# Optimization experiments

Hardware: AMD Instinct MI355X
Metric: run time of the kernel (lower is better)

## Reference

```python
import jax, jax.numpy as jnp
import numpy as np

# J2 (von Mises) elastic-plastic material, plane strain, linear isotropic hardening.
# State per integration point: committed strain (3), in-plane stress (3), out-of-plane
# stress szz (1), equivalent plastic strain eqps (1, the 'history' variable).
E_MOD = 3130.0   # Young's modulus (epoxy-like, MPa)
NU = 0.37        # Poisson ratio
SIGY0 = 64.8     # initial yield stress
HARD = 100.0     # linear hardening modulus
G_MOD = E_MOD / (2.0 * (1.0 + NU))
LAM = E_MOD * NU / ((1.0 + NU) * (1.0 - 2.0 * NU))


def _elastic_D():
    c = E_MOD / ((1.0 + NU) * (1.0 - 2.0 * NU))
    return jnp.array([[c * (1.0 - NU), c * NU, 0.0],
                      [c * NU, c * (1.0 - NU), 0.0],
                      [0.0, 0.0, G_MOD]], dtype=jnp.float32)


def _j2_step(carry, strain_t):
    # strain_t: [P,3] total strain (engineering shear) at this timestep
    eps_old, sig_old, szz_old, eqps = carry
    D = _elastic_D()
    deps = strain_t - eps_old
    sig_tr = sig_old + deps @ D.T                       # trial in-plane stress [P,3]
    szz_tr = szz_old + LAM * (deps[:, 0] + deps[:, 1])  # plane-strain out-of-plane stress
    p = (sig_tr[:, 0] + sig_tr[:, 1] + szz_tr) / 3.0
    dxx = sig_tr[:, 0] - p
    dyy = sig_tr[:, 1] - p
    dzz = szz_tr - p
    dxy = sig_tr[:, 2]
    q = jnp.sqrt(1.5 * (dxx * dxx + dyy * dyy + dzz * dzz + 2.0 * dxy * dxy) + 1e-12)
    f = q - (SIGY0 + HARD * eqps)
    dgam = jnp.where(f > 0.0, f / (3.0 * G_MOD + HARD), 0.0)  # radial return
    fac = 1.0 - 3.0 * G_MOD * dgam / q
    sig_new = jnp.stack([p + fac * dxx, p + fac * dyy, fac * dxy], axis=-1)
    szz_new = p + fac * dzz
    eqps_new = eqps + dgam  # commit()
    return (strain_t, sig_new, szz_new, eqps_new), sig_new


def reference(x, W1, W2):
    # x: [B,S,F]; W1: [ls,F] (fc1, no bias); W2: [O,ls] (softLayer: softplus-constrained weights)
    B, S, F = x.shape
    ls = W1.shape[0]
    bulk = ls // 3
    P = B * bulk
    # fc1 for all timesteps at once, then reshape to per-point strains [S, P, 3]
    strains = jnp.einsum('bsf,hf->bsh', x, W1)
    strains = strains.reshape(B, S, bulk, 3).transpose(1, 0, 2, 3).reshape(S, P, 3)
    init = (jnp.zeros((P, 3), jnp.float32), jnp.zeros((P, 3), jnp.float32),
            jnp.zeros((P,), jnp.float32), jnp.zeros((P,), jnp.float32))
    _, stresses = jax.lax.scan(_j2_step, init, strains)        # [S, P, 3]
    stresses = stresses.reshape(S, B, ls).transpose(1, 0, 2)   # [B, S, ls]
    out = jnp.einsum('bsh,oh->bso', stresses, jax.nn.softplus(W2))
    return out


def setup_inputs() -> dict:
    key = jax.random.key(0)
    k1, k2, k3 = jax.random.split(key, 3)
    B, S, F, ls, O = 128, 2048, 3, 192, 3
    x = jax.random.normal(k1, (B, S, F), dtype=jnp.float32) * 0.01  # strain-scale inputs
    W1 = jax.random.normal(k2, (ls, F), dtype=jnp.float32) / np.sqrt(F)
    W2 = jax.random.normal(k3, (O, ls), dtype=jnp.float32) / np.sqrt(ls)
    return {"x": x, "W1": W1, "W2": W2}
```

## Files before the change

### kernel.cpp

```cpp
#include <hip/hip_runtime.h>
#include <cmath>

namespace {
constexpr float kE   = 3130.0f;
constexpr float kNu  = 0.37f;
constexpr float kSy0 = 64.8f;
constexpr float kH   = 100.0f;
constexpr float kG   = kE / (2.0f * (1.0f + kNu));
constexpr float kLam = kE * kNu / ((1.0f + kNu) * (1.0f - 2.0f * kNu));
constexpr float kC   = kE / ((1.0f + kNu) * (1.0f - 2.0f * kNu));
constexpr float kC11 = kC * (1.0f - kNu);
constexpr float kC12 = kC * kNu;
constexpr float kC2  = 3.0f * kG / (3.0f * kG + kH);
constexpr float kC3  = kH / (3.0f * kG + kH);
constexpr int kS  = 2048;
constexpr int kT  = 16;
constexpr int kNBLK = kS / kT;
constexpr int kLs = 192;
constexpr float kSq15  = 1.224744871391589f;
constexpr float kSq3   = 1.732050807568877f;
constexpr float kISq15 = 1.0f / kSq15;
constexpr float kISq3  = 1.0f / kSq3;
}

typedef __fp16 half2_t __attribute__((ext_vector_type(2)));

__device__ __forceinline__ unsigned pk16(float a, float b) {
    half2_t h = __builtin_amdgcn_cvt_pkrtz(a, b);
    return __builtin_bit_cast(unsigned, h);
}
__device__ __forceinline__ float up16lo(unsigned u) {
    half2_t h = __builtin_bit_cast(half2_t, u);
    return (float)h.x;
}
__device__ __forceinline__ float up16hi(unsigned u) {
    half2_t h = __builtin_bit_cast(half2_t, u);
    return (float)h.y;
}

template<int CTRL, int RM, int BM>
__device__ __forceinline__ float dppmov(float v) {
    return __int_as_float(
        __builtin_amdgcn_update_dpp(0, __float_as_int(v), CTRL, RM, BM, false));
}
__device__ __forceinline__ float wave_sum63(float v) {
    v += dppmov<0x111, 0xf, 0xf>(v);
    v += dppmov<0x112, 0xf, 0xf>(v);
    v += dppmov<0x114, 0xf, 0xf>(v);
    v += dppmov<0x118, 0xf, 0xf>(v);
    v += dppmov<0x142, 0xa, 0xf>(v);
    v += dppmov<0x143, 0xc, 0xf>(v);
    return v;
}

__global__ __launch_bounds__(64, 1)
void j2_scan_stream(const float* __restrict__ x,
                    const float* __restrict__ W1,
                    uint4* __restrict__ ws)
{
    const int b = blockIdx.x;
    const int k = threadIdx.x;

    float wr[3][3];
#pragma unroll
    for (int j = 0; j < 3; ++j)
#pragma unroll
        for (int f = 0; f < 3; ++f)
            wr[j][f] = W1[(3 * k + j) * 3 + f];

    float g0[3], g1[3], e2s[3];
#pragma unroll
    for (int f = 0; f < 3; ++f) {
        const float e0 = kC11 * wr[0][f] + kC12 * wr[1][f];
        const float e1 = kC12 * wr[0][f] + kC11 * wr[1][f];
        const float lv = kLam * (wr[0][f] + wr[1][f]);
        g0[f]  = kSq15 * (2.0f * e0 - e1 - lv) * (1.0f / 3.0f);
        g1[f]  = kSq15 * (2.0f * e1 - e0 - lv) * (1.0f / 3.0f);
        e2s[f] = kSq3 * kG * wr[2][f];
    }

    const float* xb = x + (size_t)b * (kS * 3);

    float fw[52], fn[52];
    fw[0] = fw[1] = fw[2] = fw[3] = 0.0f;
    {
        const float4* s4 = reinterpret_cast<const float4*>(xb);
#pragma unroll
        for (int i = 0; i < 12; ++i) {
            float4 v = s4[i];
            fw[4 + 4 * i] = v.x; fw[5 + 4 * i] = v.y;
            fw[6 + 4 * i] = v.z; fw[7 + 4 * i] = v.w;
        }
    }

    float s0 = 0.f, s1 = 0.f, s2 = 0.f;
    float y = kSy0, c2y = kC2 * kSy0;
    uint4 st;

    for (int p = 0; p < kNBLK; ++p) {
        if (p + 1 < kNBLK) {
            const float4* s4 =
                reinterpret_cast<const float4*>(xb + 48 * (p + 1) - 4);
#pragma unroll
            for (int i = 0; i < 13; ++i) {
                float4 v = s4[i];
                fn[4 * i]     = v.x; fn[4 * i + 1] = v.y;
                fn[4 * i + 2] = v.z; fn[4 * i + 3] = v.w;
            }
        }
#pragma unroll
        for (int t = 0; t < kT; ++t) {
            const float d0 = fw[4 + 3 * t] - fw[1 + 3 * t];
            const float d1 = fw[5 + 3 * t] - fw[2 + 3 * t];
            const float d2 = fw[6 + 3 * t] - fw[3 + 3 * t];
            const float s0t = fmaf(g0[0], d0, fmaf(g0[1], d1, fmaf(g0[2], d2, s0)));
            const float s1t = fmaf(g1[0], d0, fmaf(g1[1], d1, fmaf(g1[2], d2, s1)));
            const float s2t = fmaf(e2s[0], d0, fmaf(e2s[1], d1, fmaf(e2s[2], d2, s2)));
            const float tt  = s0t + s1t;
            float a = fmaf(s0t, s0t, 1e-12f);
            a = fmaf(s1t, s1t, a);
            a = fmaf(s2t, s2t, a);
            const float q2  = fmaf(tt, tt, a);
            const float rq  = __builtin_amdgcn_rsqf(q2);
            const float fac = fminf(fmaf(c2y, rq, kC3), 1.0f);
            s0 = fac * s0t; s1 = fac * s1t; s2 = fac * s2t;
            const float qv = q2 * rq;
            y = fmaxf(y, fmaf(kC3, qv, c2y));
            c2y = kC2 * y;
            if ((t & 1) == 0) {
                st.x = pk16(s0, s1); st.y = pk16(s2, s2);
            } else {
                st.z = pk16(s0, s1); st.w = pk16(s2, s2);
                ws[((size_t)b * 1024 + p * 8 + (t >> 1)) * 64 + k] = st;
            }
        }
        if (p + 1 < kNBLK) {
#pragma unroll
            for (int i = 0; i < 52; ++i) fw[i] = fn[i];
        }
    }
}

__global__ __launch_bounds__(64, 1)
void j2_out_einsum(const float* __restrict__ x,
                   const float* __restrict__ W1,
                   const float* __restrict__ W2,
                   const uint4* __restrict__ ws,
                   float* __restrict__ out)
{
    const int b = blockIdx.x;
    const int tile = blockIdx.y;
    const int k = threadIdx.x;

    float wr[3][3];
#pragma unroll
    for (int j = 0; j < 3; ++j)
#pragma unroll
        for (int f = 0; f < 3; ++f)
            wr[j][f] = W1[(3 * k + j) * 3 + f];
    float mv[3];
#pragma unroll
    for (int f = 0; f < 3; ++f) {
        const float e0 = kC11 * wr[0][f] + kC12 * wr[1][f];
        const float e1 = kC12 * wr[0][f] + kC11 * wr[1][f];
        const float lv = kLam * (wr[0][f] + wr[1][f]);
        mv[f] = (e0 + e1 + lv) * (1.0f / 3.0f);
    }
    float spp[3][3], so[3];
#pragma unroll
    for (int o = 0; o < 3; ++o) {
        const float a0 = __logf(1.0f + __expf(W2[o * kLs + 3 * k + 0]));
        const float a1 = __logf(1.0f + __expf(W2[o * kLs + 3 * k + 1]));
        const float a2 = __logf(1.0f + __expf(W2[o * kLs + 3 * k + 2]));
        spp[o][0] = a0 * kISq15;
        spp[o][1] = a1 * kISq15;
        spp[o][2] = a2 * kISq3;
        so[o] = a0 + a1;
    }

    float fx[48];
    {
        const float4* s4 = reinterpret_cast<const float4*>(
            x + (size_t)b * (kS * 3) + tile * 48);
#pragma unroll
        for (int i = 0; i < 12; ++i) {
            float4 v = s4[i];
            fx[4 * i]     = v.x; fx[4 * i + 1] = v.y;
            fx[4 * i + 2] = v.z; fx[4 * i + 3] = v.w;
        }
    }

    float r[48];
#pragma unroll
    for (int j = 0; j < 8; ++j) {
        const uint4 v = ws[((size_t)b * 1024 + tile * 8 + j)* 64 + k];
#pragma unroll
        for (int h = 0; h < 2; ++h) {
            const int t = 2 * j + h;
            const unsigned pa = h ? v.z : v.x;
            const unsigned pb = h ? v.w : v.y;
            const float sx = up16lo(pa);
            const float sy = up16hi(pa);
            const float sv = up16lo(pb);
            const float pm = fmaf(mv[0], fx[3 * t],
                             fmaf(mv[1], fx[3 * t + 1], mv[2] * fx[3 * t + 2]));
#pragma unroll
            for (int o = 0; o < 3; ++o) {
                const float A = fmaf(spp[o][0], sx,
                                fmaf(spp[o][1], sy, spp[o][2] * sv));
                r[3 * t + o] = fmaf(pm, so[o], A);
            }
        }
    }
#pragma unroll
    for (int v = 0; v < 48; ++v) r[v] = wave_sum63(r[v]);
    if (k == 63) {
        float4* o4 = reinterpret_cast<float4*>(
            out + (size_t)b * (kS * 3) + tile * 48);
#pragma unroll
        for (int i = 0; i < 12; ++i)
            o4[i] = make_float4(r[4 * i], r[4 * i + 1],
                                r[4 * i + 2], r[4 * i + 3]);
    }
}

__global__ __launch_bounds__(192, 1)
void j2_pc_kernel(const float* __restrict__ x,
                  const float* __restrict__ W1,
                  const float* __restrict__ W2,
                  float* __restrict__ out)
{
    __shared__ float4 ubuf[2][kT][64];
    __shared__ float4 sgbuf[2][kT][64];

    const int b = blockIdx.x;
    const int w = threadIdx.x >> 6;
    const int k = threadIdx.x & 63;

    const float* xb = x + (size_t)b * (kS * 3);
    float* ob = out + (size_t)b * (kS * 3);

    float e0[3], e1[3], e2[3], lv[3], sp[3][3];
    if (w != 0) {
        float wr[3][3];
#pragma unroll
        for (int j = 0; j < 3; ++j)
#pragma unroll
            for (int f = 0; f < 3; ++f)
                wr[j][f] = W1[(3 * k + j) * 3 + f];
#pragma unroll
        for (int f = 0; f < 3; ++f) {
            e0[f] = kC11 * wr[0][f] + kC12 * wr[1][f];
            e1[f] = kC12 * wr[0][f] + kC11 * wr[1][f];
            e2[f] = kG * wr[2][f];
            lv[f] = kLam * (wr[0][f] + wr[1][f]);
        }
#pragma unroll
        for (int o = 0; o < 3; ++o)
#pragma unroll
            for (int j = 0; j < 3; ++j) {
                float v = W2[o * kLs + 3 * k + j];
                sp[o][j] = log1pf(expf(v));
            }
    }

    float sg0 = 0.f, sg1 = 0.f, sg2 = 0.f, szz = 0.f;
    float y = kSy0;
    const int tlo = (w == 2) ? 8 : 0;
    constexpr float kInv3GH = 1.0f / (3.0f * kG + kH);
    constexpr float k3G = 3.0f * kG;

    for (int phase = 0; phase <= kNBLK + 1; ++phase) {
        if (w == 0) {
            if (phase >= 1 && phase <= kNBLK) {
                const int blk = phase - 1, pb = blk & 1;
                float4 u[kT];
#pragma unroll
                for (int t = 0; t < kT; ++t) u[t] = ubuf[pb][t][k];
#pragma unroll
                for (int t = 0; t < kT; ++t) {
                    const float t0 = sg0 + u[t].x;
                    const float t1 = sg1 + u[t].y;
                    const float t2 = sg2 + u[t].z;
                    const float tz = szz + u[t].w;
                    const float pm  = (t0 + t1 + tz) * (1.0f / 3.0f);
                    const float dxx = t0 - pm, dyy = t1 - pm, dzz = tz - pm;
                    const float sa  = fmaf(dxx, dxx, dyy * dyy);
                    const float sb  = fmaf(dzz, dzz, (2.0f * t2) * t2);
                    const float q2  = fmaf(1.5f, sa + sb, 1e-12f);
                    const float qq  = __builtin_amdgcn_sqrtf(q2);
                    const float rq  = __builtin_amdgcn_rcpf(qq);
                    const float f   = qq - y;
                    const float dg  = (f > 0.0f) ? f * kInv3GH : 0.0f;
                    y = fmaf(kH, dg, y);
                    const float fac = fmaf(-(k3G * dg), rq, 1.0f);
                    sg0 = fmaf(fac, dxx, pm);
                    sg1 = fmaf(fac, dyy, pm);
                    sg2 = fac * t2;
                    szz = fmaf(fac, dzz, pm);
                    sgbuf[pb][t][k] = make_float4(sg0, sg1, sg2, 0.f);
                }
            }
        } else {
            if (phase < kNBLK) {
                const int p = phase, pb = p & 1;
                float xv[28];
                if (w == 1) {
                    if (p == 0) {
                        xv[0] = xv[1] = xv[2] = xv[3] = 0.f;
                        const float4* s4 = reinterpret_cast<const float4*>(xb);
#pragma unroll
                        for (int i = 0; i < 6; ++i) {
                            float4 v = s4[i];
                            xv[4 + 4 * i] = v.x; xv[5 + 4 * i] = v.y;
                            xv[6 + 4 * i] = v.z; xv[7 + 4 * i] = v.w;
                        }
                    } else {
                        const float4* s4 =
                            reinterpret_cast<const float4*>(xb + p * 48 - 4);
#pragma unroll
                        for (int i = 0; i < 7; ++i) {
                            float4 v = s4[i];
                            xv[4 * i]     = v.x; xv[4 * i + 1] = v.y;
                            xv[4 * i + 2] = v.z; xv[4 * i + 3] = v.w;
                        }
                    }
                } else {
                    const float4* s4 =
                        reinterpret_cast<const float4*>(xb + p * 48 + 20);
#pragma unroll
                    for (int i = 0; i < 7; ++i) {
                        float4 v = s4[i];
                        xv[4 * i]     = v.x; xv[4 * i + 1] = v.y;
                        xv[4 * i + 2] = v.z; xv[4 * i + 3] = v.w;
                    }
                }
                const int tbase = (w == 2) ? 8 : 0;
#pragma unroll
                for (int t = 0; t < 8; ++t) {
                    const float dx0 = xv[3 * t + 4] - xv[3 * t + 1];
                    const float dx1 = xv[3 * t + 5] - xv[3 * t + 2];
                    const float dx2 = xv[3 * t + 6] - xv[3 * t + 3];
                    float4 u;
                    u.x = fmaf(e0[0], dx0, fmaf(e0[1], dx1, e0[2] * dx2));
                    u.y = fmaf(e1[0], dx0, fmaf(e1[1], dx1, e1[2] * dx2));
                    u.z = fmaf(e2[0], dx0, fmaf(e2[1], dx1, e2[2] * dx2));
                    u.w = fmaf(lv[0], dx0, fmaf(lv[1], dx1, lv[2] * dx2));
                    ubuf[pb][tbase + t][k] = u;
                }
            }
            if (phase >= 2) {
                const int q = phase - 2, qb = q & 1;
                const int tbase = tlo;
                float r[24];
#pragma unroll
                for (int t = 0; t < 8; ++t) {
                    float4 s = sgbuf[qb][tbase + t][k];
                    r[3 * t]     = fmaf(sp[0][0], s.x, fmaf(sp[0][1], s.y, sp[0][2] * s.z));
                    r[3 * t + 1] = fmaf(sp[1][0], s.x, fmaf(sp[1][1], s.y, sp[1][2] * s.z));
                    r[3 * t + 2] = fmaf(sp[2][0], s.x, fmaf(sp[2][1], s.y, sp[2][2] * s.z));
                }
#pragma unroll
                for (int v = 0; v < 24; ++v) r[v] = wave_sum63(r[v]);
                if (k == 63) {
                    float4* o4 = reinterpret_cast<float4*>(ob + q * 48 + tbase * 3);
#pragma unroll
                    for (int i = 0; i < 6; ++i)
                        o4[i] = make_float4(r[4 * i], r[4 * i + 1],
                                            r[4 * i + 2], r[4 * i + 3]);
                }
            }
        }
        __syncthreads();
    }
}

extern "C" void kernel_launch(void* const* d_in, const int* in_sizes, int n_in,
                              void* d_out, int out_size, void* d_ws, size_t ws_size,
                              hipStream_t stream) {
    const float* x  = (const float*)d_in[0];
    const float* W1 = (const float*)d_in[1];
    const float* W2 = (const float*)d_in[2];
    float* out = (float*)d_out;

    const size_t need = (size_t)128 * 1024 * 64 * sizeof(uint4);
    if (ws_size >= need) {
        uint4* ws = (uint4*)d_ws;
        j2_scan_stream<<<dim3(128), dim3(64), 0, stream>>>(x, W1, ws);
        j2_out_einsum<<<dim3(128, 128), dim3(64), 0, stream>>>(x, W1, W2, ws, out);
    } else {
        j2_pc_kernel<<<dim3(128), dim3(192), 0, stream>>>(x, W1, W2, out);
    }
}
```

Before: 169.3 us.

## Precompute duplicated strain deltas and use packed FP32 math in scan

Adds a preprocessing kernel that computes per-timestep input differences and stores each one twice in a global buffer. The serial scan kernel then reads these with double-buffered vector loads and computes the two deviatoric stress components with packed v_pk_fma_f32 instructions. It also reorders the q² reduction to shorten the dependency chain. The aim is to cut per-step latency on the sequential critical path, at the cost of an extra kernel launch and about 6 MB of extra global memory traffic.

```diff
diff --git a/kernel.cpp b/kernel.cpp
--- a/kernel.cpp
+++ b/kernel.cpp
@@ -24,6 +24,8 @@
 }
 
 typedef __fp16 half2_t __attribute__((ext_vector_type(2)));
+typedef float f2_t __attribute__((ext_vector_type(2)));
+typedef float f4_t __attribute__((ext_vector_type(4)));
 
 __device__ __forceinline__ unsigned pk16(float a, float b) {
     half2_t h = __builtin_amdgcn_cvt_pkrtz(a, b);
@@ -36,6 +38,15 @@
 __device__ __forceinline__ float up16hi(unsigned u) {
     half2_t h = __builtin_bit_cast(half2_t, u);
     return (float)h.y;
+}
+
+__device__ __forceinline__ f2_t pkmul(f2_t a, f2_t b) {
+    f2_t d;
+    asm("v_pk_mul_f32 %0, %1, %2" : "=v"(d) : "v"(a), "v"(b));
+    return d;
+}
+__device__ __forceinline__ void pkfma(f2_t& acc, f2_t a, f2_t b) {
+    asm("v_pk_fma_f32 %0, %1, %2, %0" : "+v"(acc) : "v"(a), "v"(b));
 }
 
 template<int CTRL, int RM, int BM>
@@ -53,10 +64,26 @@
     return v;
 }
 
+__device__ __align__(16) float g_dxd[128 * 2048 * 6];
+
+__global__ __launch_bounds__(256, 4)
+void j2_dx_dup(const float* __restrict__ x)
+{
+    const int gid = blockIdx.x * 256 + threadIdx.x;
+    const int t = gid & 2047;
+    const float* xe = x + (size_t)gid * 3;
+    const float a0 = xe[0], a1 = xe[1], a2 = xe[2];
+    float p0 = 0.f, p1 = 0.f, p2 = 0.f;
+    if (t != 0) { p0 = xe[-3]; p1 = xe[-2]; p2 = xe[-1]; }
+    const float d0 = a0 - p0, d1 = a1 - p1, d2 = a2 - p2;
+    float2* o = reinterpret_cast<float2*>(g_dxd + (size_t)gid * 6);
+    o[0] = make_float2(d0, d0);
+    o[1] = make_float2(d1, d1);
+    o[2] = make_float2(d2, d2);
+}
+
 __global__ __launch_bounds__(64, 1)
-void j2_scan_stream(const float* __restrict__ x,
-                    const float* __restrict__ W1,
-                    uint4* __restrict__ ws)
+void j2_scan2(const float* __restrict__ W1, uint4* __restrict__ ws)
 {
     const int b = blockIdx.x;
     const int k = threadIdx.x;
@@ -68,77 +95,82 @@
         for (int f = 0; f < 3; ++f)
             wr[j][f] = W1[(3 * k + j) * 3 + f];
 
-    float g0[3], g1[3], e2s[3];
+    f2_t g01[3];
+    float e2s[3];
 #pragma unroll
     for (int f = 0; f < 3; ++f) {
         const float e0 = kC11 * wr[0][f] + kC12 * wr[1][f];
         const float e1 = kC12 * wr[0][f] + kC11 * wr[1][f];
         const float lv = kLam * (wr[0][f] + wr[1][f]);
-        g0[f]  = kSq15 * (2.0f * e0 - e1 - lv) * (1.0f / 3.0f);
-        g1[f]  = kSq15 * (2.0f * e1 - e0 - lv) * (1.0f / 3.0f);
-        e2s[f] = kSq3 * kG * wr[2][f];
-    }
-
-    const float* xb = x + (size_t)b * (kS * 3);
-
-    float fw[52], fn[52];
-    fw[0] = fw[1] = fw[2] = fw[3] = 0.0f;
-    {
-        const float4* s4 = reinterpret_cast<const float4*>(xb);
-#pragma unroll
-        for (int i = 0; i < 12; ++i) {
-            float4 v = s4[i];
-            fw[4 + 4 * i] = v.x; fw[5 + 4 * i] = v.y;
-            fw[6 + 4 * i] = v.z; fw[7 + 4 * i] = v.w;
-        }
-    }
+        g01[f][0] = kSq15 * (2.0f * e0 - e1 - lv) * (1.0f / 3.0f);
+        g01[f][1] = kSq15 * (2.0f * e1 - e0 - lv) * (1.0f / 3.0f);
+        e2s[f]    = kSq3 * kG * wr[2][f];
+    }
+
+    const float* db = g_dxd + (size_t)b * (2048 * 6);
 
     float s0 = 0.f, s1 = 0.f, s2 = 0.f;
     float y = kSy0, c2y = kC2 * kSy0;
-    uint4 st;
-
-    for (int p = 0; p < kNBLK; ++p) {
-        if (p + 1 < kNBLK) {
-            const float4* s4 =
-                reinterpret_cast<const float4*>(xb + 48 * (p + 1) - 4);
-#pragma unroll
-            for (int i = 0; i < 13; ++i) {
-                float4 v = s4[i];
-                fn[4 * i]     = v.x; fn[4 * i + 1] = v.y;
-                fn[4 * i + 2] = v.z; fn[4 * i + 3] = v.w;
-            }
-        }
-#pragma unroll
-        for (int t = 0; t < kT; ++t) {
-            const float d0 = fw[4 + 3 * t] - fw[1 + 3 * t];
-            const float d1 = fw[5 + 3 * t] - fw[2 + 3 * t];
-            const float d2 = fw[6 + 3 * t] - fw[3 + 3 * t];
-            const float s0t = fmaf(g0[0], d0, fmaf(g0[1], d1, fmaf(g0[2], d2, s0)));
-            const float s1t = fmaf(g1[0], d0, fmaf(g1[1], d1, fmaf(g1[2], d2, s1)));
-            const float s2t = fmaf(e2s[0], d0, fmaf(e2s[1], d1, fmaf(e2s[2], d2, s2)));
-            const float tt  = s0t + s1t;
-            float a = fmaf(s0t, s0t, 1e-12f);
-            a = fmaf(s1t, s1t, a);
-            a = fmaf(s2t, s2t, a);
-            const float q2  = fmaf(tt, tt, a);
-            const float rq  = __builtin_amdgcn_rsqf(q2);
-            const float fac = fminf(fmaf(c2y, rq, kC3), 1.0f);
-            s0 = fac * s0t; s1 = fac * s1t; s2 = fac * s2t;
-            const float qv = q2 * rq;
-            y = fmaxf(y, fmaf(kC3, qv, c2y));
-            c2y = kC2 * y;
-            if ((t & 1) == 0) {
-                st.x = pk16(s0, s1); st.y = pk16(s2, s2);
-            } else {
-                st.z = pk16(s0, s1); st.w = pk16(s2, s2);
-                ws[((size_t)b * 1024 + p * 8 + (t >> 1)) * 64 + k] = st;
-            }
-        }
-        if (p + 1 < kNBLK) {
-#pragma unroll
-            for (int i = 0; i < 52; ++i) fw[i] = fn[i];
-        }
-    }
+
+    auto step = [&](f2_t d0, f2_t d1, f2_t d2) -> uint2 {
+        f2_t u = pkmul(g01[0], d0);
+        pkfma(u, g01[1], d1);
+        pkfma(u, g01[2], d2);
+        float u2 = fmaf(e2s[1], d1[0], e2s[0] * d0[0]);
+        u2 = fmaf(e2s[2], d2[0], u2);
+        const float s0t = s0 + u[0];
+        const float s1t = s1 + u[1];
+        const float s2t = s2 + u2;
+        const float tt  = s0t + s1t;
+        const float c1  = fmaf(s0t, s0t, 1e-12f);
+        const float cc  = fmaf(tt, tt, s2t * s2t);
+        const float q2  = fmaf(s1t, s1t, c1) + cc;
+        const float rq  = __builtin_amdgcn_rsqf(q2);
+        const float fac = fminf(fmaf(c2y, rq, kC3), 1.0f);
+        s0 = fac * s0t; s1 = fac * s1t; s2 = fac * s2t;
+        const float qv = q2 * rq;
+        y = fmaxf(y, fmaf(kC3, qv, c2y));
+        c2y = kC2 * y;
+        return make_uint2(pk16(s0, s1), pk16(s2, s2));
+    };
+
+    f4_t buf0[24], buf1[24];
+
+#define LOADB(dst, p)                                                       \
+    {                                                                       \
+        const f4_t* s_ = reinterpret_cast<const f4_t*>(db + (p) * 96);      \
+        _Pragma("unroll")                                                   \
+        for (int i_ = 0; i_ < 24; ++i_) dst[i_] = s_[i_];                   \
+    }
+
+#define BODY(buf, p)                                                        \
+    {                                                                       \
+        _Pragma("unroll")                                                   \
+        for (int i = 0; i < 8; ++i) {                                       \
+            const f4_t Fa = buf[3 * i], Fb = buf[3 * i + 1],                \
+                       Fc = buf[3 * i + 2];                                 \
+            uint4 st;                                                       \
+            uint2 e = step(__builtin_shufflevector(Fa, Fa, 0, 1),           \
+                           __builtin_shufflevector(Fa, Fa, 2, 3),           \
+                           __builtin_shufflevector(Fb, Fb, 0, 1));          \
+            st.x = e.x; st.y = e.y;                                         \
+            uint2 o = step(__builtin_shufflevector(Fb, Fb, 2, 3),           \
+                           __builtin_shufflevector(Fc, Fc, 0, 1),           \
+                           __builtin_shufflevector(Fc, Fc, 2, 3));          \
+            st.z = o.x; st.w = o.y;                                         \
+            ws[((size_t)b * 1024 + (p) * 8 + i) * 64 + k] = st;             \
+        }                                                                   \
+    }
+
+    LOADB(buf0, 0);
+    for (int pp = 0; pp < kNBLK; pp += 2) {
+        LOADB(buf1, pp + 1);
+        BODY(buf0, pp);
+        if (pp + 2 < kNBLK) LOADB(buf0, pp + 2);
+        BODY(buf1, pp + 1);
+    }
+#undef LOADB
+#undef BODY
 }
 
 __global__ __launch_bounds__(64, 1)
@@ -193,7 +225,7 @@
     float r[48];
 #pragma unroll
     for (int j = 0; j < 8; ++j) {
-        const uint4 v = ws[((size_t)b * 1024 + tile * 8 + j)* 64 + k];
+        const uint4 v = ws[((size_t)b * 1024 + tile * 8 + j) * 64 + k];
 #pragma unroll
         for (int h = 0; h < 2; ++h) {
             const int t = 2 * j + h;
@@ -386,7 +418,8 @@
     const size_t need = (size_t)128 * 1024 * 64 * sizeof(uint4);
     if (ws_size >= need) {
         uint4* ws = (uint4*)d_ws;
-        j2_scan_stream<<<dim3(128), dim3(64), 0, stream>>>(x, W1, ws);
+        j2_dx_dup<<<dim3(1024), dim3(256), 0, stream>>>(x);
+        j2_scan2<<<dim3(128), dim3(64), 0, stream>>>(W1, ws);
         j2_out_einsum<<<dim3(128, 128), dim3(64), 0, stream>>>(x, W1, W2, ws, out);
     } else {
         j2_pc_kernel<<<dim3(128), dim3(192), 0, stream>>>(x, W1, W2, out);
```

Result: slower. 303.6 us (+79.4%).

## Split J2 scan across 4 lanes per point with DPP reduction and precomputed strain deltas

Applied to the files above, without the earlier changes.

Adds a pre-pass kernel that writes strain increments into a global buffer. The scan kernel now gives each material point four lanes (deviatoric xx, yy, xy and zz components) and forms the squared norm with quad DPP adds. It also launches 4x more blocks, so the serial recurrence gets more parallelism and its per-lane register and FMA count drops. The workspace layout changes to per-component packed pairs of timesteps, and the out-einsum unpacking is changed to match. The cost is an extra kernel launch plus the global round-trip for the deltas, and each lane's serial chain now carries DPP latency.

```diff
diff --git a/kernel.cpp b/kernel.cpp
--- a/kernel.cpp
+++ b/kernel.cpp
@@ -24,6 +24,7 @@
 }
 
 typedef __fp16 half2_t __attribute__((ext_vector_type(2)));
+typedef float f4_t __attribute__((ext_vector_type(4)));
 
 __device__ __forceinline__ unsigned pk16(float a, float b) {
     half2_t h = __builtin_amdgcn_cvt_pkrtz(a, b);
@@ -52,92 +53,101 @@
     v += dppmov<0x143, 0xc, 0xf>(v);
     return v;
 }
+template<int CTRL>
+__device__ __forceinline__ float qdpp(float v) {
+    return __int_as_float(
+        __builtin_amdgcn_update_dpp(0, __float_as_int(v), CTRL, 0xF, 0xF, true));
+}
+
+__device__ __align__(16) float g_dx[128 * 2048 * 3];
+
+__global__ __launch_bounds__(256, 4)
+void j2_dx(const float* __restrict__ x)
+{
+    const int gid = blockIdx.x * 256 + threadIdx.x;
+    const int t = gid & 2047;
+    const float* xe = x + (size_t)gid * 3;
+    const float a0 = xe[0], a1 = xe[1], a2 = xe[2];
+    float p0 = 0.f, p1 = 0.f, p2 = 0.f;
+    if (t != 0) { p0 = xe[-3]; p1 = xe[-2]; p2 = xe[-1]; }
+    float* o = g_dx + (size_t)gid * 3;
+    o[0] = a0 - p0; o[1] = a1 - p1; o[2] = a2 - p2;
+}
 
 __global__ __launch_bounds__(64, 1)
-void j2_scan_stream(const float* __restrict__ x,
-                    const float* __restrict__ W1,
-                    uint4* __restrict__ ws)
+void j2_scan4(const float* __restrict__ W1, unsigned* __restrict__ ws32)
 {
-    const int b = blockIdx.x;
-    const int k = threadIdx.x;
-
-    float wr[3][3];
-#pragma unroll
-    for (int j = 0; j < 3; ++j)
-#pragma unroll
-        for (int f = 0; f < 3; ++f)
-            wr[j][f] = W1[(3 * k + j) * 3 + f];
-
-    float g0[3], g1[3], e2s[3];
+    const int b   = blockIdx.x;
+    const int qtr = blockIdx.y;
+    const int ln  = threadIdx.x;
+    const int kc  = ln >> 2;
+    const int c   = ln & 3;
+    const int kg  = qtr * 16 + kc;
+
+    float gv[3];
 #pragma unroll
     for (int f = 0; f < 3; ++f) {
-        const float e0 = kC11 * wr[0][f] + kC12 * wr[1][f];
-        const float e1 = kC12 * wr[0][f] + kC11 * wr[1][f];
-        const float lv = kLam * (wr[0][f] + wr[1][f]);
-        g0[f]  = kSq15 * (2.0f * e0 - e1 - lv) * (1.0f / 3.0f);
-        g1[f]  = kSq15 * (2.0f * e1 - e0 - lv) * (1.0f / 3.0f);
-        e2s[f] = kSq3 * kG * wr[2][f];
-    }
-
-    const float* xb = x + (size_t)b * (kS * 3);
-
-    float fw[52], fn[52];
-    fw[0] = fw[1] = fw[2] = fw[3] = 0.0f;
-    {
-        const float4* s4 = reinterpret_cast<const float4*>(xb);
-#pragma unroll
-        for (int i = 0; i < 12; ++i) {
-            float4 v = s4[i];
-            fw[4 + 4 * i] = v.x; fw[5 + 4 * i] = v.y;
-            fw[6 + 4 * i] = v.z; fw[7 + 4 * i] = v.w;
-        }
-    }
-
-    float s0 = 0.f, s1 = 0.f, s2 = 0.f;
-    float y = kSy0, c2y = kC2 * kSy0;
-    uint4 st;
-
-    for (int p = 0; p < kNBLK; ++p) {
-        if (p + 1 < kNBLK) {
-            const float4* s4 =
-                reinterpret_cast<const float4*>(xb + 48 * (p + 1) - 4);
-#pragma unroll
-            for (int i = 0; i < 13; ++i) {
-                float4 v = s4[i];
-                fn[4 * i]     = v.x; fn[4 * i + 1] = v.y;
-                fn[4 * i + 2] = v.z; fn[4 * i + 3] = v.w;
-            }
-        }
+        const float w0 = W1[(3 * kg + 0) * 3 + f];
+        const float w1 = W1[(3 * kg + 1) * 3 + f];
+        const float w2 = W1[(3 * kg + 2) * 3 + f];
+        const float e0 = kC11 * w0 + kC12 * w1;
+        const float e1 = kC12 * w0 + kC11 * w1;
+        const float lv = kLam * (w0 + w1);
+        const float g0 = kSq15 * (2.0f * e0 - e1 - lv) * (1.0f / 3.0f);
+        const float g1 = kSq15 * (2.0f * e1 - e0 - lv) * (1.0f / 3.0f);
+        const float g2 = kSq3 * kG * w2;
+        const float gz = -(g0 + g1);
+        gv[f] = (c == 0) ? g0 : (c == 1) ? g1 : (c == 2) ? g2 : gz;
+    }
+
+    const float* db = g_dx + (size_t)b * (kS * 3);
+    unsigned* wsb = ws32 + (size_t)b * 1024 * 256 + qtr * 64 + ln;
+
+    float s = 0.f, y = kSy0, c2y = kC2 * kSy0;
+
+    auto loadw = [&](f4_t* dst, int p) {
+        const f4_t* s4 = reinterpret_cast<const f4_t*>(db + p * 48);
+#pragma unroll
+        for (int i = 0; i < 12; ++i) dst[i] = s4[i];
+    };
+
+    auto body = [&](const f4_t* Wd, int p) {
+        float u[kT];
 #pragma unroll
         for (int t = 0; t < kT; ++t) {
-            const float d0 = fw[4 + 3 * t] - fw[1 + 3 * t];
-            const float d1 = fw[5 + 3 * t] - fw[2 + 3 * t];
-            const float d2 = fw[6 + 3 * t] - fw[3 + 3 * t];
-            const float s0t = fmaf(g0[0], d0, fmaf(g0[1], d1, fmaf(g0[2], d2, s0)));
-            const float s1t = fmaf(g1[0], d0, fmaf(g1[1], d1, fmaf(g1[2], d2, s1)));
-            const float s2t = fmaf(e2s[0], d0, fmaf(e2s[1], d1, fmaf(e2s[2], d2, s2)));
-            const float tt  = s0t + s1t;
-            float a = fmaf(s0t, s0t, 1e-12f);
-            a = fmaf(s1t, s1t, a);
-            a = fmaf(s2t, s2t, a);
-            const float q2  = fmaf(tt, tt, a);
-            const float rq  = __builtin_amdgcn_rsqf(q2);
+            const float d0 = Wd[(3 * t + 0) >> 2][(3 * t + 0) & 3];
+            const float d1 = Wd[(3 * t + 1) >> 2][(3 * t + 1) & 3];
+            const float d2 = Wd[(3 * t + 2) >> 2][(3 * t + 2) & 3];
+            u[t] = fmaf(gv[0], d0, fmaf(gv[1], d1, gv[2] * d2));
+        }
+        float se = 0.f;
+#pragma unroll
+        for (int t = 0; t < kT; ++t) {
+            const float st = s + u[t];
+            float pp = fmaf(st, st, 2.5e-13f);
+            pp += qdpp<0xB1>(pp);
+            pp += qdpp<0x4E>(pp);
+            const float rq  = __builtin_amdgcn_rsqf(pp);
             const float fac = fminf(fmaf(c2y, rq, kC3), 1.0f);
-            s0 = fac * s0t; s1 = fac * s1t; s2 = fac * s2t;
-            const float qv = q2 * rq;
+            s = fac * st;
+            const float qv = pp * rq;
             y = fmaxf(y, fmaf(kC3, qv, c2y));
             c2y = kC2 * y;
             if ((t & 1) == 0) {
-                st.x = pk16(s0, s1); st.y = pk16(s2, s2);
+                se = s;
             } else {
-                st.z = pk16(s0, s1); st.w = pk16(s2, s2);
-                ws[((size_t)b * 1024 + p * 8 + (t >> 1)) * 64 + k] = st;
-            }
-        }
-        if (p + 1 < kNBLK) {
-#pragma unroll
-            for (int i = 0; i < 52; ++i) fw[i] = fn[i];
-        }
+                wsb[(size_t)(p * 8 + (t >> 1)) * 256] = pk16(se, s);
+            }
+        }
+    };
+
+    f4_t A[12], B[12];
+    loadw(A, 0);
+    for (int p = 0; p < kNBLK; p += 2) {
+        loadw(B, p + 1);
+        body(A, p);
+        if (p + 2 < kNBLK) loadw(A, p + 2);
+        body(B, p + 1);
     }
 }
 
@@ -193,15 +203,13 @@
     float r[48];
 #pragma unroll
     for (int j = 0; j < 8; ++j) {
-        const uint4 v = ws[((size_t)b * 1024 + tile * 8 + j)* 64 + k];
+        const uint4 v = ws[((size_t)b * 1024 + tile * 8 + j) * 64 + k];
 #pragma unroll
         for (int h = 0; h < 2; ++h) {
             const int t = 2 * j + h;
-            const unsigned pa = h ? v.z : v.x;
-            const unsigned pb = h ? v.w : v.y;
-            const float sx = up16lo(pa);
-            const float sy = up16hi(pa);
-            const float sv = up16lo(pb);
+            const float sx = h ? up16hi(v.x) : up16lo(v.x);
+            const float sy = h ? up16hi(v.y) : up16lo(v.y);
+            const float sv = h ? up16hi(v.z) : up16lo(v.z);
             const float pm = fmaf(mv[0], fx[3 * t],
                              fmaf(mv[1], fx[3 * t + 1], mv[2] * fx[3 * t + 2]));
 #pragma unroll
@@ -385,9 +393,10 @@
 
     const size_t need = (size_t)128 * 1024 * 64 * sizeof(uint4);
     if (ws_size >= need) {
-        uint4* ws = (uint4*)d_ws;
-        j2_scan_stream<<<dim3(128), dim3(64), 0, stream>>>(x, W1, ws);
-        j2_out_einsum<<<dim3(128, 128), dim3(64), 0, stream>>>(x, W1, W2, ws, out);
+        j2_dx<<<dim3(1024), dim3(256), 0, stream>>>(x);
+        j2_scan4<<<dim3(128, 4), dim3(64), 0, stream>>>(W1, (unsigned*)d_ws);
+        j2_out_einsum<<<dim3(128, 128), dim3(64), 0, stream>>>(
+            x, W1, W2, (const uint4*)d_ws, out);
     } else {
         j2_pc_kernel<<<dim3(128), dim3(192), 0, stream>>>(x, W1, W2, out);
     }
```

Result: faster. 150.1 us, median of 2 (-11.3%).
